# Performance work log

Measured on AMD Instinct MI355X. Metric: run time of the kernel, lower is better.

## Reference

```python
import jax, jax.numpy as jnp
import numpy as np

HEADS = 16
HEAD_DIM = 64
HIDDEN = HEADS * HEAD_DIM  # 1024
COMPRESSION = 1.0  # concat([o, p], -1) forces compressed seq len == T, i.e. scale 1
LN_EPS = 1e-5


def _interp_linear_seq(x, scale):
    # F.interpolate(mode='linear', align_corners=False) along the sequence axis.
    # x: [B, T, C] -> [B, int(T*scale), C]
    T = x.shape[1]
    S = int(T * scale)
    src = (jnp.arange(S, dtype=jnp.float32) + 0.5) / scale - 0.5
    src = jnp.clip(src, 0.0, T - 1)
    lo = jnp.floor(src).astype(jnp.int32)
    hi = jnp.minimum(lo + 1, T - 1)
    w = (src - lo.astype(jnp.float32))[None, :, None]
    return x[:, lo] * (1.0 - w) + x[:, hi] * w


def _rotary(x):
    # rotate-half rotary embedding; x: [B, S, h, d]
    S, d = x.shape[1], x.shape[3]
    inv_freq = 1.0 / (10000.0 ** (jnp.arange(0, d, 2, dtype=jnp.float32) / d))
    ang = jnp.arange(S, dtype=jnp.float32)[:, None] * inv_freq  # [S, d/2]
    cos = jnp.cos(ang)[None, :, None, :]
    sin = jnp.sin(ang)[None, :, None, :]
    x1, x2 = jnp.split(x, 2, axis=-1)
    return jnp.concatenate([x1 * cos - x2 * sin, x1 * sin + x2 * cos], axis=-1)


def setup_inputs() -> dict:
    key = jax.random.key(0)
    ks = jax.random.split(key, 4)
    B, T = 4, 2048
    x = jax.random.normal(ks[0], (B, T, HIDDEN), dtype=jnp.float32)
    ln_gamma = jnp.ones((HIDDEN,), dtype=jnp.float32)
    ln_beta = jnp.zeros((HIDDEN,), dtype=jnp.float32)
    w_in = jax.random.normal(ks[1], (HIDDEN, 7 * HIDDEN), dtype=jnp.float32) * (HIDDEN ** -0.5)
    w_out = jax.random.normal(ks[2], (5 * HIDDEN, HIDDEN), dtype=jnp.float32) * ((5 * HIDDEN) ** -0.5)
    b_out = jnp.zeros((HIDDEN,), dtype=jnp.float32)
    return {"x": x, "ln_gamma": ln_gamma, "ln_beta": ln_beta,
            "w_in": w_in, "w_out": w_out, "b_out": b_out}


def reference(x, ln_gamma, ln_beta, w_in, w_out, b_out):
    B, T, _ = x.shape
    # LayerNorm
    mu = jnp.mean(x, axis=-1, keepdims=True)
    var = jnp.mean(jnp.square(x - mu), axis=-1, keepdims=True)
    xn = (x - mu) / jnp.sqrt(var + LN_EPS) * ln_gamma + ln_beta
    # fused QKVP projection (no bias)
    qkvp = xn @ w_in  # [B, T, 7*HIDDEN]
    q, k, v, p = jnp.split(qkvp, [HIDDEN, 2 * HIDDEN, 3 * HIDDEN], axis=-1)
    # linear-interpolation compression of k, v, p along the sequence axis
    k = _interp_linear_seq(k, COMPRESSION)
    v = _interp_linear_seq(v, COMPRESSION)
    p = _interp_linear_seq(p, COMPRESSION)
    S = k.shape[1]
    q = q.reshape(B, T, HEADS, HEAD_DIM)
    k = k.reshape(B, S, HEADS, HEAD_DIM)
    v = v.reshape(B, S, HEADS, HEAD_DIM)
    q = _rotary(q)
    k = _rotary(k)
    # manual softmax attention (no mask in the original)
    a = jnp.einsum('bihd,bjhd->bhij', q, k) * (HEAD_DIM ** -0.5)
    a = jax.nn.softmax(a, axis=-1)
    o = jnp.einsum('bhij,bjhd->bihd', a, v).reshape(B, T, HIDDEN)
    # GELU side branch (torch F.gelu default = exact erf gelu)
    p = jax.nn.gelu(p, approximate=False)
    return jnp.concatenate([o, p], axis=-1) @ w_out + b_out
```

## Files before the change

kernel.cpp:

```cpp
#include <hip/hip_runtime.h>
#include <hip/hip_bf16.h>
#include <math.h>

typedef short bf16x8 __attribute__((ext_vector_type(8)));
typedef float f32x4 __attribute__((ext_vector_type(4)));

#define HEADS 16
#define HDIM 64
#define HID 1024
#define B_ 4
#define T_ 2048
#define BT_ (B_*T_)
#define N1 (7*HID)
#define K2 (5*HID)

#define SM_SCALE_LOG2E 0.18033688011111793f

__device__ __forceinline__ float bf2f(unsigned short u) {
  union { unsigned int i; float f; } c; c.i = ((unsigned int)u) << 16; return c.f;
}
__device__ __forceinline__ unsigned short f2bf(float f) {
  __hip_bfloat16 h = __float2bfloat16(f);
  return __builtin_bit_cast(unsigned short, h);
}
__device__ __forceinline__ float gelu_fast(float x) {
  float y = 0.7978845608028654f * (x + 0.044715f * x * x * x);
  float e = exp2f(y * 2.8853900817779268f);
  float t = 1.f - 2.f / (e + 1.f);
  return 0.5f * x * (1.f + t);
}

__global__ __launch_bounds__(256) void tcast_kernel(const float* __restrict__ in,
                                                    unsigned short* __restrict__ out,
                                                    int R, int C) {
  __shared__ float tile[64][65];
  int tx = threadIdx.x & 63;
  int ty = threadIdx.x >> 6;
  long r0 = (long)blockIdx.y * 64;
  long c0 = (long)blockIdx.x * 64;
#pragma unroll
  for (int i = 0; i < 16; i++) {
    int r = ty + i * 4;
    tile[r][tx] = in[(r0 + r) * C + c0 + tx];
  }
  __syncthreads();
#pragma unroll
  for (int i = 0; i < 16; i++) {
    int rr = ty + i * 4;
    out[(c0 + rr) * R + r0 + tx] = f2bf(tile[tx][rr]);
  }
}

__global__ __launch_bounds__(256) void ln_kernel(const float* __restrict__ x,
                                                 const float* __restrict__ g,
                                                 const float* __restrict__ b,
                                                 unsigned short* __restrict__ xn) {
  int row = blockIdx.x, tid = threadIdx.x;
  float4 v = reinterpret_cast<const float4*>(x + (long)row * HID)[tid];
  float s = v.x + v.y + v.z + v.w;
  float sq = v.x * v.x + v.y * v.y + v.z * v.z + v.w * v.w;
#pragma unroll
  for (int off = 32; off > 0; off >>= 1) { s += __shfl_down(s, off); sq += __shfl_down(sq, off); }
  __shared__ float red[8];
  int wid = tid >> 6, lane = tid & 63;
  if (lane == 0) { red[wid] = s; red[4 + wid] = sq; }
  __syncthreads();
  if (tid == 0) {
    red[0] = red[0] + red[1] + red[2] + red[3];
    red[4] = red[4] + red[5] + red[6] + red[7];
  }
  __syncthreads();
  float mean = red[0] * (1.f / HID);
  float var  = red[4] * (1.f / HID) - mean * mean;
  float rstd = rsqrtf(var + 1e-5f);
  float4 gv = reinterpret_cast<const float4*>(g)[tid];
  float4 bv = reinterpret_cast<const float4*>(b)[tid];
  ushort4 o;
  o.x = f2bf((v.x - mean) * rstd * gv.x + bv.x);
  o.y = f2bf((v.y - mean) * rstd * gv.y + bv.y);
  o.z = f2bf((v.z - mean) * rstd * gv.z + bv.z);
  o.w = f2bf((v.w - mean) * rstd * gv.w + bv.w);
  reinterpret_cast<ushort4*>(xn + (long)row * HID)[tid] = o;
}

__device__ __forceinline__ void gemm_core32(const unsigned short* __restrict__ A,
                                            const unsigned short* __restrict__ BT,
                                            unsigned short* As, unsigned short* Bs,
                                            int K, int lda, int ldb,
                                            long row0, long col0,
                                            int lane, int wid, f32x4 (&acc)[4][4]) {
  int l15 = lane & 15, lq = lane >> 4;
  int srow = lane >> 2;
  int schnk = lane & 3;
  int r0s = wid * 32 + srow;
  int r1s = r0s + 16;
  int slot0 = schnk ^ ((r0s >> 1) & 3);
  int slot1 = schnk ^ ((r1s >> 1) & 3);
  const unsigned short* a0 = A + (row0 + r0s) * (long)lda + schnk * 8;
  const unsigned short* a1 = A + (row0 + r1s) * (long)lda + schnk * 8;
  const unsigned short* b0 = BT + (col0 + r0s) * (long)ldb + schnk * 8;
  const unsigned short* b1 = BT + (col0 + r1s) * (long)ldb + schnk * 8;
  bf16x8 ar0 = *reinterpret_cast<const bf16x8*>(a0);
  bf16x8 ar1 = *reinterpret_cast<const bf16x8*>(a1);
  bf16x8 br0 = *reinterpret_cast<const bf16x8*>(b0);
  bf16x8 br1 = *reinterpret_cast<const bf16x8*>(b1);
  int wm = (wid & 1) * 64, wn = (wid >> 1) * 64;
  for (int k0 = 0; k0 < K; k0 += 32) {
    *reinterpret_cast<bf16x8*>(&As[r0s * 32 + slot0 * 8]) = ar0;
    *reinterpret_cast<bf16x8*>(&As[r1s * 32 + slot1 * 8]) = ar1;
    *reinterpret_cast<bf16x8*>(&Bs[r0s * 32 + slot0 * 8]) = br0;
    *reinterpret_cast<bf16x8*>(&Bs[r1s * 32 + slot1 * 8]) = br1;
    if (k0 + 32 < K) {
      ar0 = *reinterpret_cast<const bf16x8*>(a0 + k0 + 32);
      ar1 = *reinterpret_cast<const bf16x8*>(a1 + k0 + 32);
      br0 = *reinterpret_cast<const bf16x8*>(b0 + k0 + 32);
      br1 = *reinterpret_cast<const bf16x8*>(b1 + k0 + 32);
    }
    __syncthreads();
    bf16x8 af[4], bfv[4];
#pragma unroll
    for (int m = 0; m < 4; m++) {
      int r = wm + m * 16 + l15;
      af[m] = *reinterpret_cast<const bf16x8*>(&As[r * 32 + (lq ^ ((r >> 1) & 3)) * 8]);
    }
#pragma unroll
    for (int n = 0; n < 4; n++) {
      int r = wn + n * 16 + l15;
      bfv[n] = *reinterpret_cast<const bf16x8*>(&Bs[r * 32 + (lq ^ ((r >> 1) & 3)) * 8]);
    }
#pragma unroll
    for (int m = 0; m < 4; m++)
#pragma unroll
      for (int n = 0; n < 4; n++)
        acc[m][n] = __builtin_amdgcn_mfma_f32_16x16x32_bf16(af[m], bfv[n], acc[m][n], 0, 0, 0);
    __syncthreads();
  }
}

__global__ __launch_bounds__(256) void gemm1_fused(const unsigned short* __restrict__ A,
                                                   const unsigned short* __restrict__ BT,
                                                   unsigned short* __restrict__ q_r,
                                                   unsigned short* __restrict__ k_r,
                                                   unsigned short* __restrict__ v_t,
                                                   unsigned short* __restrict__ C5) {
  __shared__ unsigned short As[128 * 32];
  __shared__ unsigned short Bs[128 * 32];
  __shared__ unsigned short Vt[4][64 * 72];
  int tid = threadIdx.x, lane = tid & 63, wid = tid >> 6;
  long row0 = (long)blockIdx.y * 128;
  long col0 = (long)blockIdx.x * 128;
  f32x4 acc[4][4] = {};
  gemm_core32(A, BT, As, Bs, HID, HID, HID, row0, col0, lane, wid, acc);

  int wm = (wid & 1) * 64, wn = (wid >> 1) * 64;
  long row_base = row0 + wm;
  int b = (int)(row_base >> 11);
  int t_base = (int)(row_base & 2047);
  int col_base = (int)col0 + wn;
  int region = col_base >> 10;
  int l15 = lane & 15, lq = lane >> 4;

  if (region <= 1) {
    unsigned short* dst = (region == 0) ? q_r : k_r;
    float osc = (region == 0) ? SM_SCALE_LOG2E : 1.0f;
    int head = (col_base & 1023) >> 6;
    long obase = (long)(b * 16 + head) * T_ * 64;
    float fr[2];
    fr[0] = __expf(-(float)l15 * 0.28782313662425572f);
    fr[1] = __expf(-(float)(16 + l15) * 0.28782313662425572f);
#pragma unroll
    for (int m = 0; m < 4; m++) {
#pragma unroll
      for (int j = 0; j < 4; j++) {
        int t = t_base + m * 16 + lq * 4 + j;
#pragma unroll
        for (int n = 0; n < 2; n++) {
          float sn, cs;
          __sincosf((float)t * fr[n], &sn, &cs);
          float xl = acc[m][n][j], xh = acc[m][n + 2][j];
          int d = n * 16 + l15;
          dst[obase + (long)t * 64 + d]      = f2bf((xl * cs - xh * sn) * osc);
          dst[obase + (long)t * 64 + d + 32] = f2bf((xl * sn + xh * cs) * osc);
        }
      }
    }
  } else if (region == 2) {
    int head = (col_base & 1023) >> 6;
    unsigned short* vt = &Vt[wid][0];
#pragma unroll
    for (int m = 0; m < 4; m++)
#pragma unroll
      for (int n = 0; n < 4; n++)
#pragma unroll
        for (int j = 0; j < 4; j++)
          vt[(n * 16 + l15) * 72 + m * 16 + lq * 4 + j] = f2bf(acc[m][n][j]);
    long obase = (long)(b * 16 + head) * 64 * T_;
#pragma unroll
    for (int i = 0; i < 8; i++) {
      int d = i * 8 + (lane >> 3);
      int tl = (lane & 7) * 8;
      bf16x8 v = *reinterpret_cast<const bf16x8*>(&vt[d * 72 + tl]);
      *reinterpret_cast<bf16x8*>(v_t + obase + (long)d * T_ + t_base + tl) = v;
    }
  } else {
    int colp = col_base - 3 * HID;
#pragma unroll
    for (int m = 0; m < 4; m++) {
#pragma unroll
      for (int j = 0; j < 4; j++) {
        long row = row_base + m * 16 + lq * 4 + j;
#pragma unroll
        for (int n = 0; n < 4; n++)
          C5[row * K2 + HID + colp + n * 16 + l15] = f2bf(gelu_fast(acc[m][n][j]));
      }
    }
  }
}

__global__ __launch_bounds__(256) void gemm_bt(const unsigned short* __restrict__ A,
                                               const unsigned short* __restrict__ BT,
                                               float* __restrict__ Cout,
                                               const float* __restrict__ bias,
                                               int K, int lda, int ldb, int ldc) {
  __shared__ unsigned short As[128 * 32];
  __shared__ unsigned short Bs[128 * 32];
  int tid = threadIdx.x, lane = tid & 63, wid = tid >> 6;
  long row0 = (long)blockIdx.y * 128;
  long col0 = (long)blockIdx.x * 128;
  f32x4 acc[4][4] = {};
  gemm_core32(A, BT, As, Bs, K, lda, ldb, row0, col0, lane, wid, acc);
  int wm = (wid & 1) * 64, wn = (wid >> 1) * 64;
#pragma unroll
  for (int m = 0; m < 4; m++) {
#pragma unroll
    for (int n = 0; n < 4; n++) {
      long r = row0 + wm + m * 16 + (lane >> 4) * 4;
      long c = col0 + wn + n * 16 + (lane & 15);
#pragma unroll
      for (int j = 0; j < 4; j++)
        Cout[(r + j) * (long)ldc + c] = acc[m][n][j] + bias[c];
    }
  }
}

__global__ __launch_bounds__(256) void attn_kernel(const unsigned short* __restrict__ q_r,
                                                   const unsigned short* __restrict__ k_r,
                                                   const unsigned short* __restrict__ v_t,
                                                   unsigned short* __restrict__ C5) {
  int qt = blockIdx.x;
  int bh = blockIdx.y;
  int b = bh >> 4, h = bh & 15;
  int tid = threadIdx.x, lane = tid & 63, wid = tid >> 6;
  int l15 = lane & 15, lq = lane >> 4;
  __shared__ unsigned short Ks[64 * 64];
  __shared__ unsigned short Vts[64 * 64];
  __shared__ unsigned short Ps[4][32 * 64];

  const unsigned short* qbase = q_r + ((long)bh * T_ + qt * 128 + wid * 32) * 64;
  bf16x8 aq[2][2];
#pragma unroll
  for (int m = 0; m < 2; m++)
#pragma unroll
    for (int kk = 0; kk < 2; kk++)
      aq[m][kk] = *reinterpret_cast<const bf16x8*>(
          qbase + (m * 16 + l15) * 64 + kk * 32 + lq * 8);

  f32x4 o_acc[2][4] = {};
  float l_run[2][4] = {};

  const unsigned short* kbase = k_r + (long)bh * T_ * 64;
  const unsigned short* vbase = v_t + (long)bh * 64 * T_;
  int srow = lane >> 3;
  int schnk = lane & 7;
  int slot = schnk ^ srow;
  unsigned short* Pw = &Ps[wid][0];

  bf16x8 kreg[2], vreg[2];
#pragma unroll
  for (int i = 0; i < 2; i++) {
    int c = wid * 2 + i;
    kreg[i] = *reinterpret_cast<const bf16x8*>(kbase + c * 512 + lane * 8);
    vreg[i] = *reinterpret_cast<const bf16x8*>(vbase + (long)(c * 8 + srow) * T_ + schnk * 8);
  }

  for (int kt = 0; kt < 32; kt++) {
#pragma unroll
    for (int i = 0; i < 2; i++) {
      int r = (wid * 2 + i) * 8 + srow;
      *reinterpret_cast<bf16x8*>(&Ks[r * 64 + slot * 8])  = kreg[i];
      *reinterpret_cast<bf16x8*>(&Vts[r * 64 + slot * 8]) = vreg[i];
    }
    if (kt < 31) {
#pragma unroll
      for (int i = 0; i < 2; i++) {
        int c = wid * 2 + i;
        kreg[i] = *reinterpret_cast<const bf16x8*>(kbase + (kt + 1) * 4096 + c * 512 + lane * 8);
        vreg[i] = *reinterpret_cast<const bf16x8*>(vbase + (long)(c * 8 + srow) * T_ + (kt + 1) * 64 + schnk * 8);
      }
    }
    __syncthreads();
    f32x4 s[2][4] = {};
#pragma unroll
    for (int n = 0; n < 4; n++) {
      int krow = n * 16 + l15;
      bf16x8 bk[2];
#pragma unroll
      for (int kk = 0; kk < 2; kk++)
        bk[kk] = *reinterpret_cast<const bf16x8*>(
            &Ks[krow * 64 + ((kk * 4 + lq) ^ (krow & 7)) * 8]);
#pragma unroll
      for (int m = 0; m < 2; m++)
#pragma unroll
        for (int kk = 0; kk < 2; kk++)
          s[m][n] = __builtin_amdgcn_mfma_f32_16x16x32_bf16(aq[m][kk], bk[kk], s[m][n], 0, 0, 0);
    }
#pragma unroll
    for (int m = 0; m < 2; m++)
#pragma unroll
      for (int n = 0; n < 4; n++)
#pragma unroll
        for (int j = 0; j < 4; j++) {
          float p = exp2f(s[m][n][j]);
          l_run[m][j] += p;
          int prow = m * 16 + lq * 4 + j;
          int pcol = n * 16 + l15;
          Pw[prow * 64 + (((pcol >> 3) ^ (prow & 7)) << 3) + (pcol & 7)] = f2bf(p);
        }
    bf16x8 ap[2][2];
#pragma unroll
    for (int m = 0; m < 2; m++)
#pragma unroll
      for (int kk = 0; kk < 2; kk++) {
        int prow = m * 16 + l15;
        ap[m][kk] = *reinterpret_cast<const bf16x8*>(
            &Pw[prow * 64 + (((kk * 4 + lq) ^ (prow & 7)) << 3)]);
      }
#pragma unroll
    for (int n = 0; n < 4; n++) {
      int vrow = n * 16 + l15;
      bf16x8 bv[2];
#pragma unroll
      for (int kk = 0; kk < 2; kk++)
        bv[kk] = *reinterpret_cast<const bf16x8*>(
            &Vts[vrow * 64 + ((kk * 4 + lq) ^ (vrow & 7)) * 8]);
#pragma unroll
      for (int m = 0; m < 2; m++)
#pragma unroll
        for (int kk = 0; kk < 2; kk++)
          o_acc[m][n] = __builtin_amdgcn_mfma_f32_16x16x32_bf16(ap[m][kk], bv[kk], o_acc[m][n], 0, 0, 0);
    }
    __syncthreads();
  }
#pragma unroll
  for (int m = 0; m < 2; m++)
#pragma unroll
    for (int j = 0; j < 4; j++) {
      float l = l_run[m][j];
      l += __shfl_xor(l, 1);
      l += __shfl_xor(l, 2);
      l += __shfl_xor(l, 4);
      l += __shfl_xor(l, 8);
      float inv = 1.0f / l;
      int tl = qt * 128 + wid * 32 + m * 16 + lq * 4 + j;
      long row = (long)b * T_ + tl;
#pragma unroll
      for (int n = 0; n < 4; n++) {
        int col = h * 64 + n * 16 + l15;
        C5[row * K2 + col] = f2bf(o_acc[m][n][j] * inv);
      }
    }
}

extern "C" void kernel_launch(void* const* d_in, const int* in_sizes, int n_in,
                              void* d_out, int out_size, void* d_ws, size_t ws_size,
                              hipStream_t stream) {
  const float* x     = (const float*)d_in[0];
  const float* g     = (const float*)d_in[1];
  const float* be    = (const float*)d_in[2];
  const float* w_in  = (const float*)d_in[3];
  const float* w_out = (const float*)d_in[4];
  const float* b_out = (const float*)d_in[5];
  float* out = (float*)d_out;

  char* ws = (char*)d_ws;
  size_t off = 0;
  auto alloc = [&](size_t bytes) {
    void* p = ws + off;
    off += (bytes + 255) & ~(size_t)255;
    return p;
  };
  unsigned short* xn     = (unsigned short*)alloc((size_t)BT_ * HID * 2);
  unsigned short* w_inT  = (unsigned short*)alloc((size_t)N1 * HID * 2);
  unsigned short* w_outT = (unsigned short*)alloc((size_t)HID * K2 * 2);
  unsigned short* q_rb   = (unsigned short*)alloc((size_t)BT_ * HID * 2);
  unsigned short* k_rb   = (unsigned short*)alloc((size_t)BT_ * HID * 2);
  unsigned short* v_tb   = (unsigned short*)alloc((size_t)BT_ * HID * 2);
  unsigned short* C5     = (unsigned short*)alloc((size_t)BT_ * K2 * 2);

  tcast_kernel<<<dim3(N1 / 64, HID / 64), 256, 0, stream>>>(w_in, w_inT, HID, N1);
  tcast_kernel<<<dim3(HID / 64, K2 / 64), 256, 0, stream>>>(w_out, w_outT, K2, HID);
  ln_kernel<<<BT_, 256, 0, stream>>>(x, g, be, xn);
  gemm1_fused<<<dim3(N1 / 128, BT_ / 128), 256, 0, stream>>>(xn, w_inT, q_rb, k_rb, v_tb, C5);
  attn_kernel<<<dim3(T_ / 128, 64), 256, 0, stream>>>(q_rb, k_rb, v_tb, C5);
  gemm_bt<<<dim3(HID / 128, BT_ / 128), 256, 0, stream>>>(C5, w_outT, out, b_out,
                                                          K2, K2, K2, HID);
}
```

Measured before the change: 461.4 us.

## Double-buffer LDS tiles in GEMM core to halve barriers per k-step

Replaces the single-buffered LDS GEMM mainloop with a ping-pong double buffer. Each k-step now reads fragments from the current buffer, writes the next tile into the other buffer and prefetches the tile after that from global memory, all before the MFMAs, with only one barrier per step. The Vt transpose scratch in gemm1 is aliased onto the same shared array once the mainloop is done. This doubles the LDS tile footprint, which may lower occupancy, and the extra prefetch stage raises register pressure.

```diff
diff --git a/kernel.cpp b/kernel.cpp
--- a/kernel.cpp
+++ b/kernel.cpp
@@ -83,12 +83,12 @@
   reinterpret_cast<ushort4*>(xn + (long)row * HID)[tid] = o;
 }
 
-__device__ __forceinline__ void gemm_core32(const unsigned short* __restrict__ A,
-                                            const unsigned short* __restrict__ BT,
-                                            unsigned short* As, unsigned short* Bs,
-                                            int K, int lda, int ldb,
-                                            long row0, long col0,
-                                            int lane, int wid, f32x4 (&acc)[4][4]) {
+__device__ __forceinline__ void gemm_core_db(const unsigned short* __restrict__ A,
+                                             const unsigned short* __restrict__ BT,
+                                             unsigned short* As, unsigned short* Bs,
+                                             int K, int lda, int ldb,
+                                             long row0, long col0,
+                                             int lane, int wid, f32x4 (&acc)[4][4]) {
   int l15 = lane & 15, lq = lane >> 4;
   int srow = lane >> 2;
   int schnk = lane & 3;
@@ -100,33 +100,52 @@
   const unsigned short* a1 = A + (row0 + r1s) * (long)lda + schnk * 8;
   const unsigned short* b0 = BT + (col0 + r0s) * (long)ldb + schnk * 8;
   const unsigned short* b1 = BT + (col0 + r1s) * (long)ldb + schnk * 8;
+  int wm = (wid & 1) * 64, wn = (wid >> 1) * 64;
+  int NT = K / 32;
+
   bf16x8 ar0 = *reinterpret_cast<const bf16x8*>(a0);
   bf16x8 ar1 = *reinterpret_cast<const bf16x8*>(a1);
   bf16x8 br0 = *reinterpret_cast<const bf16x8*>(b0);
   bf16x8 br1 = *reinterpret_cast<const bf16x8*>(b1);
-  int wm = (wid & 1) * 64, wn = (wid >> 1) * 64;
-  for (int k0 = 0; k0 < K; k0 += 32) {
-    *reinterpret_cast<bf16x8*>(&As[r0s * 32 + slot0 * 8]) = ar0;
-    *reinterpret_cast<bf16x8*>(&As[r1s * 32 + slot1 * 8]) = ar1;
-    *reinterpret_cast<bf16x8*>(&Bs[r0s * 32 + slot0 * 8]) = br0;
-    *reinterpret_cast<bf16x8*>(&Bs[r1s * 32 + slot1 * 8]) = br1;
-    if (k0 + 32 < K) {
-      ar0 = *reinterpret_cast<const bf16x8*>(a0 + k0 + 32);
-      ar1 = *reinterpret_cast<const bf16x8*>(a1 + k0 + 32);
-      br0 = *reinterpret_cast<const bf16x8*>(b0 + k0 + 32);
-      br1 = *reinterpret_cast<const bf16x8*>(b1 + k0 + 32);
-    }
-    __syncthreads();
+  *reinterpret_cast<bf16x8*>(&As[r0s * 32 + slot0 * 8]) = ar0;
+  *reinterpret_cast<bf16x8*>(&As[r1s * 32 + slot1 * 8]) = ar1;
+  *reinterpret_cast<bf16x8*>(&Bs[r0s * 32 + slot0 * 8]) = br0;
+  *reinterpret_cast<bf16x8*>(&Bs[r1s * 32 + slot1 * 8]) = br1;
+  ar0 = *reinterpret_cast<const bf16x8*>(a0 + 32);
+  ar1 = *reinterpret_cast<const bf16x8*>(a1 + 32);
+  br0 = *reinterpret_cast<const bf16x8*>(b0 + 32);
+  br1 = *reinterpret_cast<const bf16x8*>(b1 + 32);
+  __syncthreads();
+
+  int cur = 0;
+  for (int t = 0; t < NT; t++) {
+    const unsigned short* Asr = As + cur * 4096;
+    const unsigned short* Bsr = Bs + cur * 4096;
     bf16x8 af[4], bfv[4];
 #pragma unroll
     for (int m = 0; m < 4; m++) {
       int r = wm + m * 16 + l15;
-      af[m] = *reinterpret_cast<const bf16x8*>(&As[r * 32 + (lq ^ ((r >> 1) & 3)) * 8]);
+      af[m] = *reinterpret_cast<const bf16x8*>(&Asr[r * 32 + (lq ^ ((r >> 1) & 3)) * 8]);
     }
 #pragma unroll
     for (int n = 0; n < 4; n++) {
       int r = wn + n * 16 + l15;
-      bfv[n] = *reinterpret_cast<const bf16x8*>(&Bs[r * 32 + (lq ^ ((r >> 1) & 3)) * 8]);
+      bfv[n] = *reinterpret_cast<const bf16x8*>(&Bsr[r * 32 + (lq ^ ((r >> 1) & 3)) * 8]);
+    }
+    if (t + 1 < NT) {
+      unsigned short* Asw = As + (cur ^ 1) * 4096;
+      unsigned short* Bsw = Bs + (cur ^ 1) * 4096;
+      *reinterpret_cast<bf16x8*>(&Asw[r0s * 32 + slot0 * 8]) = ar0;
+      *reinterpret_cast<bf16x8*>(&Asw[r1s * 32 + slot1 * 8]) = ar1;
+      *reinterpret_cast<bf16x8*>(&Bsw[r0s * 32 + slot0 * 8]) = br0;
+      *reinterpret_cast<bf16x8*>(&Bsw[r1s * 32 + slot1 * 8]) = br1;
+    }
+    if (t + 2 < NT) {
+      long ko = (long)(t + 2) * 32;
+      ar0 = *reinterpret_cast<const bf16x8*>(a0 + ko);
+      ar1 = *reinterpret_cast<const bf16x8*>(a1 + ko);
+      br0 = *reinterpret_cast<const bf16x8*>(b0 + ko);
+      br1 = *reinterpret_cast<const bf16x8*>(b1 + ko);
     }
 #pragma unroll
     for (int m = 0; m < 4; m++)
@@ -134,6 +153,7 @@
       for (int n = 0; n < 4; n++)
         acc[m][n] = __builtin_amdgcn_mfma_f32_16x16x32_bf16(af[m], bfv[n], acc[m][n], 0, 0, 0);
     __syncthreads();
+    cur ^= 1;
   }
 }
 
@@ -143,14 +163,14 @@
                                                    unsigned short* __restrict__ k_r,
                                                    unsigned short* __restrict__ v_t,
                                                    unsigned short* __restrict__ C5) {
-  __shared__ unsigned short As[128 * 32];
-  __shared__ unsigned short Bs[128 * 32];
-  __shared__ unsigned short Vt[4][64 * 72];
+  __shared__ unsigned short smem[18432];
+  unsigned short* As = smem;
+  unsigned short* Bs = smem + 8192;
   int tid = threadIdx.x, lane = tid & 63, wid = tid >> 6;
   long row0 = (long)blockIdx.y * 128;
   long col0 = (long)blockIdx.x * 128;
   f32x4 acc[4][4] = {};
-  gemm_core32(A, BT, As, Bs, HID, HID, HID, row0, col0, lane, wid, acc);
+  gemm_core_db(A, BT, As, Bs, HID, HID, HID, row0, col0, lane, wid, acc);
 
   int wm = (wid & 1) * 64, wn = (wid >> 1) * 64;
   long row_base = row0 + wm;
@@ -186,7 +206,7 @@
     }
   } else if (region == 2) {
     int head = (col_base & 1023) >> 6;
-    unsigned short* vt = &Vt[wid][0];
+    unsigned short* vt = smem + wid * 4608;
 #pragma unroll
     for (int m = 0; m < 4; m++)
 #pragma unroll
@@ -222,13 +242,14 @@
                                                float* __restrict__ Cout,
                                                const float* __restrict__ bias,
                                                int K, int lda, int ldb, int ldc) {
-  __shared__ unsigned short As[128 * 32];
-  __shared__ unsigned short Bs[128 * 32];
+  __shared__ unsigned short smem[16384];
+  unsigned short* As = smem;
+  unsigned short* Bs = smem + 8192;
   int tid = threadIdx.x, lane = tid & 63, wid = tid >> 6;
   long row0 = (long)blockIdx.y * 128;
   long col0 = (long)blockIdx.x * 128;
   f32x4 acc[4][4] = {};
-  gemm_core32(A, BT, As, Bs, K, lda, ldb, row0, col0, lane, wid, acc);
+  gemm_core_db(A, BT, As, Bs, K, lda, ldb, row0, col0, lane, wid, acc);
   int wm = (wid & 1) * 64, wn = (wid >> 1) * 64;
 #pragma unroll
   for (int m = 0; m < 4; m++) {
```

Measured after the change: 444.5 us. -3.7%, faster.
